# Kernel tuning notes

Hardware: AMD Instinct MI355X
Metric: run time of the kernel (lower is better)

The kernel has to match this reference:

```python
import jax, jax.numpy as jnp
import numpy as np

EPS = 1e-5
K = 20
THRESH = 0.5

def _bn_relu(x, g, b, m, v):
    # eval-mode BatchNorm1d followed by ReLU
    return jax.nn.relu(g * (x - m) * jax.lax.rsqrt(v + EPS) + b)

def setup_inputs() -> dict:
    key = jax.random.key(0)
    ks = jax.random.split(key, 16)
    T, C, CI, E, NC = 16384, 256, 8, 5, 13
    B, N = 2, T // 2
    inp = {
        "f_sem": jax.random.normal(ks[0], (T, C), jnp.float32),
        "f_ins": jax.random.normal(ks[1], (T, CI), jnp.float32),
        # equal-size, sorted batch assignment (2 clouds of 8192 points)
        "batch": jnp.repeat(jnp.arange(B, dtype=jnp.int64), N),
        # semantic_adaptation_fc: Linear(C,C) + BN + ReLU
        "W_sem": jax.random.normal(ks[2], (C, C), jnp.float32) * (1.0 / np.sqrt(C)),
        "b_sem": jnp.zeros((C,), jnp.float32),
        "g_sem": jnp.ones((C,), jnp.float32),
        "beta_sem": jnp.zeros((C,), jnp.float32),
        "m_sem": jax.random.normal(ks[3], (C,), jnp.float32) * 0.1,
        "v_sem": jax.random.uniform(ks[4], (C,), jnp.float32, 0.5, 1.5),
        # inst_fc: Linear(8,C) + BN + ReLU
        "W_ins": jax.random.normal(ks[5], (CI, C), jnp.float32) * (1.0 / np.sqrt(CI)),
        "b_ins": jnp.zeros((C,), jnp.float32),
        "g_ins": jnp.ones((C,), jnp.float32),
        "beta_ins": jnp.zeros((C,), jnp.float32),
        "m_ins": jax.random.normal(ks[6], (C,), jnp.float32) * 0.1,
        "v_ins": jax.random.uniform(ks[7], (C,), jnp.float32, 0.5, 1.5),
        # instance_embedding_fc: plain Linear(C,E)
        "W_emb": jax.random.normal(ks[8], (C, E), jnp.float32) * (1.0 / np.sqrt(C)),
        "b_emb": jnp.zeros((E,), jnp.float32),
        # classifier_fc: plain Linear(C,NC)
        "W_cls": jax.random.normal(ks[9], (C, NC), jnp.float32) * (1.0 / np.sqrt(C)),
        "b_cls": jnp.zeros((NC,), jnp.float32),
    }
    return inp

def _instance_fusion(e_ins, f_sem, batch):
    # assumes sorted batch with equal-size segments (enforced by setup_inputs)
    T, C = f_sem.shape
    B = int(batch[-1]) + 1
    N = T // B
    e = e_ins.reshape(B, N, -1)
    f = f_sem.reshape(B, N, C)
    # squared Euclidean pairwise distances per cloud: [B, N, N]
    sq = jnp.sum(e * e, axis=-1)
    d2 = sq[:, :, None] + sq[:, None, :] - 2.0 * jnp.einsum("bnd,bmd->bnm", e, e)
    d2 = jnp.maximum(d2, 0.0)
    neg_vals, idx = jax.lax.top_k(-d2, K)          # k smallest distances, [B,N,K]
    within = (-neg_vals) <= THRESH * THRESH        # distance <= threshold
    self_idx = jnp.broadcast_to(jnp.arange(N)[None, :, None], idx.shape)
    col = jnp.where(within, idx, self_idx)         # fall back to self outside threshold
    neigh = jax.vmap(lambda fb, cb: fb[cb])(f, col)  # [B,N,K,C]
    return jnp.max(neigh, axis=2).reshape(T, C)      # scatter-max == max over neighbors

def reference(f_sem, f_ins, batch,
              W_sem, b_sem, g_sem, beta_sem, m_sem, v_sem,
              W_ins, b_ins, g_ins, beta_ins, m_ins, v_ins,
              W_emb, b_emb, W_cls, b_cls):
    f_sem_prime = _bn_relu(f_sem @ W_sem + b_sem, g_sem, beta_sem, m_sem, v_sem)
    f_ins_h = _bn_relu(f_ins @ W_ins + b_ins, g_ins, beta_ins, m_ins, v_ins)
    f_sins = f_ins_h + f_sem_prime
    e_ins = f_sins @ W_emb + b_emb
    f_isem = _instance_fusion(e_ins, f_sem, batch)
    p_sem = f_isem @ W_cls + b_cls
    return (p_sem, e_ins)
```

## Files before the change

kernel.cpp:

```cpp
#include <hip/hip_runtime.h>
#include <math.h>

#define T 16384
#define C 256
#define CI 8
#define EDIM 5
#define NC 13
#define NPTS 8192
#define KNN 20
#define CAP 256
#define FR 32
#define FRPB 8

typedef float f4v __attribute__((ext_vector_type(4)));
typedef _Float16 h8 __attribute__((ext_vector_type(8)));

__global__ __launch_bounds__(256) void front_kernel(
    const float* __restrict__ f_sem, const float* __restrict__ f_ins,
    const float* __restrict__ W_sem, const float* __restrict__ b_sem,
    const float* __restrict__ g_sem, const float* __restrict__ beta_sem,
    const float* __restrict__ m_sem, const float* __restrict__ v_sem,
    const float* __restrict__ W_ins, const float* __restrict__ b_ins,
    const float* __restrict__ g_ins, const float* __restrict__ beta_ins,
    const float* __restrict__ m_ins, const float* __restrict__ v_ins,
    const float* __restrict__ W_emb, const float* __restrict__ b_emb,
    float* __restrict__ eA, double* __restrict__ eD,
    float* __restrict__ out_e)
{
    __shared__ __align__(16) _Float16 sAh[FR][264];
    __shared__ __align__(16) _Float16 sAl[FR][264];
    __shared__ float bnA1[C], bnB1[C], bnA2[C], bnB2[C];
    __shared__ float weL[C][EDIM];
    __shared__ float lfi[FR][CI];
    __shared__ float sP[4][FR][EDIM];

    const int tid = threadIdx.x;
    const int rowBase = blockIdx.x * FR;

    #pragma unroll
    for (int i = 0; i < 8; i++) {
        const int idx = tid + 256 * i;
        const int g = idx * 4;
        const int row = g >> 8, k = g & 255;
        const float4 v = *(const float4*)(f_sem + (size_t)rowBase * C + g);
        const float vv[4] = {v.x, v.y, v.z, v.w};
        #pragma unroll
        for (int q = 0; q < 4; q++) {
            const _Float16 h = (_Float16)vv[q];
            sAh[row][k + q] = h;
            sAl[row][k + q] = (_Float16)(vv[q] - (float)h);
        }
    }
    {
        const int c = tid;
        const float rs1 = 1.0f / sqrtf(v_sem[c] + 1e-5f);
        const float A1 = g_sem[c] * rs1;
        bnA1[c] = A1;
        bnB1[c] = A1 * (b_sem[c] - m_sem[c]) + beta_sem[c];
        const float rs2 = 1.0f / sqrtf(v_ins[c] + 1e-5f);
        const float A2 = g_ins[c] * rs2;
        bnA2[c] = A2;
        bnB2[c] = A2 * (b_ins[c] - m_ins[c]) + beta_ins[c];
        #pragma unroll
        for (int j = 0; j < EDIM; j++) weL[c][j] = W_emb[c * EDIM + j];
    }
    if (tid < FR * CI) lfi[tid >> 3][tid & 7] = f_ins[rowBase * CI + tid];
    __syncthreads();

    const int w = tid >> 6, lane = tid & 63;
    const int r16 = lane & 15, kq = lane >> 4;
    const int n0 = 64 * w;

    f4v acc[2][4];
    #pragma unroll
    for (int mi = 0; mi < 2; mi++)
        #pragma unroll
        for (int ni = 0; ni < 4; ni++) acc[mi][ni] = (f4v){0.f, 0.f, 0.f, 0.f};

    for (int kt = 0; kt < 8; kt++) {
        const int koff = 32 * kt + 8 * kq;
        const h8 ah0 = *(const h8*)&sAh[r16][koff];
        const h8 ah1 = *(const h8*)&sAh[r16 + 16][koff];
        const h8 al0 = *(const h8*)&sAl[r16][koff];
        const h8 al1 = *(const h8*)&sAl[r16 + 16][koff];
        #pragma unroll
        for (int ni = 0; ni < 4; ni++) {
            const float* wp = W_sem + (size_t)koff * C + (n0 + 16 * ni + r16);
            float wf[8];
            #pragma unroll
            for (int j = 0; j < 8; j++) wf[j] = wp[(size_t)j * C];
            h8 bh, bl;
            #pragma unroll
            for (int j = 0; j < 8; j++) {
                const _Float16 h = (_Float16)wf[j];
                bh[j] = h;
                bl[j] = (_Float16)(wf[j] - (float)h);
            }
            acc[0][ni] = __builtin_amdgcn_mfma_f32_16x16x32_f16(ah0, bh, acc[0][ni], 0, 0, 0);
            acc[1][ni] = __builtin_amdgcn_mfma_f32_16x16x32_f16(ah1, bh, acc[1][ni], 0, 0, 0);
            acc[0][ni] = __builtin_amdgcn_mfma_f32_16x16x32_f16(al0, bh, acc[0][ni], 0, 0, 0);
            acc[1][ni] = __builtin_amdgcn_mfma_f32_16x16x32_f16(al1, bh, acc[1][ni], 0, 0, 0);
            acc[0][ni] = __builtin_amdgcn_mfma_f32_16x16x32_f16(ah0, bl, acc[0][ni], 0, 0, 0);
            acc[1][ni] = __builtin_amdgcn_mfma_f32_16x16x32_f16(ah1, bl, acc[1][ni], 0, 0, 0);
        }
    }

    f4v prow, pcol;
    {
        const f4v z = {0.f, 0.f, 0.f, 0.f};
        h8 ra, rb, ca, cb;
        #pragma unroll
        for (int j = 0; j < 8; j++) {
            ra[j] = (_Float16)(float)r16;
            rb[j] = (_Float16)((kq == 0 && j == 0) ? 1.0f : 0.0f);
            ca[j] = rb[j];
            cb[j] = ra[j];
        }
        prow = __builtin_amdgcn_mfma_f32_16x16x32_f16(ra, rb, z, 0, 0, 0);
        pcol = __builtin_amdgcn_mfma_f32_16x16x32_f16(ca, cb, z, 0, 0, 0);
    }
    const int colm = (int)pcol[0];
    int rloc[4];
    #pragma unroll
    for (int r = 0; r < 4; r++) rloc[r] = (int)prow[r];

    float p[2][4][EDIM];
    #pragma unroll
    for (int mi = 0; mi < 2; mi++)
        #pragma unroll
        for (int r = 0; r < 4; r++)
            #pragma unroll
            for (int j = 0; j < EDIM; j++) p[mi][r][j] = 0.f;

    #pragma unroll
    for (int ni = 0; ni < 4; ni++) {
        const int c = n0 + 16 * ni + colm;
        const float A1 = bnA1[c], B1 = bnB1[c];
        const float A2 = bnA2[c], B2 = bnB2[c];
        float wi[CI], we[EDIM];
        #pragma unroll
        for (int k = 0; k < CI; k++) wi[k] = W_ins[k * C + c];
        #pragma unroll
        for (int j = 0; j < EDIM; j++) we[j] = weL[c][j];
        #pragma unroll
        for (int mi = 0; mi < 2; mi++)
            #pragma unroll
            for (int r = 0; r < 4; r++) {
                const int row = 16 * mi + rloc[r];
                float x2 = 0.f;
                #pragma unroll
                for (int k = 0; k < CI; k++) x2 = fmaf(lfi[row][k], wi[k], x2);
                const float h1 = fmaxf(fmaf(A1, acc[mi][ni][r], B1), 0.f);
                const float h2 = fmaxf(fmaf(A2, x2, B2), 0.f);
                const float s = h1 + h2;
                #pragma unroll
                for (int j = 0; j < EDIM; j++) p[mi][r][j] = fmaf(s, we[j], p[mi][r][j]);
            }
    }

    #pragma unroll
    for (int off = 1; off < 16; off <<= 1)
        #pragma unroll
        for (int mi = 0; mi < 2; mi++)
            #pragma unroll
            for (int r = 0; r < 4; r++)
                #pragma unroll
                for (int j = 0; j < EDIM; j++)
                    p[mi][r][j] += __shfl_xor(p[mi][r][j], off);

    if (r16 == 0) {
        #pragma unroll
        for (int mi = 0; mi < 2; mi++)
            #pragma unroll
            for (int r = 0; r < 4; r++)
                #pragma unroll
                for (int j = 0; j < EDIM; j++)
                    sP[w][16 * mi + rloc[r]][j] = p[mi][r][j];
    }
    __syncthreads();

    if (tid < FR) {
        const int row = rowBase + tid;
        double sq = 0.0;
        #pragma unroll
        for (int j = 0; j < EDIM; j++) {
            const float s = ((sP[0][tid][j] + sP[1][tid][j]) +
                             (sP[2][tid][j] + sP[3][tid][j])) + b_emb[j];
            const double ed = (double)s;
            eD[(size_t)row * 8 + j] = ed;
            sq = fma(ed, ed, sq);
            eA[(size_t)row * 8 + j] = s;
            out_e[(size_t)row * EDIM + j] = s;
        }
        eD[(size_t)row * 8 + 5] = sq;
        eA[(size_t)row * 8 + 5] = (float)sq;
        eA[(size_t)row * 8 + 6] = 0.f;
        eA[(size_t)row * 8 + 7] = 0.f;
    }
}

__device__ __attribute__((noinline)) float4 rescan_topk(
    const float* __restrict__ eA, const float* __restrict__ f_sem,
    const float* __restrict__ reRow, int cbase, int lane)
{
    float re0 = reRow[0], re1 = reRow[1], re2 = reRow[2];
    float re3 = reRow[3], re4 = reRow[4], sqF = reRow[5];
    float4 mx = make_float4(-3.4e38f, -3.4e38f, -3.4e38f, -3.4e38f);
    long long last = -1;
    for (int sel = 0; sel < KNN; sel++) {
        long long best = 0x7fffffffffffffffLL;
        for (int cb = 0; cb < NPTS; cb += 64) {
            const int j = cbase + cb + lane;
            const float4 ea = *(const float4*)(eA + (size_t)j * 8);
            const float2 eb = *(const float2*)(eA + (size_t)j * 8 + 4);
            float dot = re0 * ea.x;
            dot = fmaf(re1, ea.y, dot); dot = fmaf(re2, ea.z, dot);
            dot = fmaf(re3, ea.w, dot); dot = fmaf(re4, eb.x, dot);
            const float d2 = fmaxf((sqF + eb.y) - 2.f * dot, 0.f);
            long long key = (((long long)__float_as_uint(d2)) << 32)
                            | (unsigned int)(cb + lane);
            if (key <= last) key = 0x7fffffffffffffffLL;
            if (key < best) best = key;
        }
        #pragma unroll
        for (int off = 32; off; off >>= 1) {
            const long long o = __shfl_xor(best, off);
            if (o < best) best = o;
        }
        last = best;
        const int idx = (int)(best & 0xffffffffLL);
        const float4 fv = *(const float4*)(f_sem + (size_t)(cbase + idx) * C + lane * 4);
        mx.x = fmaxf(mx.x, fv.x); mx.y = fmaxf(mx.y, fv.y);
        mx.z = fmaxf(mx.z, fv.z); mx.w = fmaxf(mx.w, fv.w);
    }
    return mx;
}

__global__ __launch_bounds__(256) void knn_kernel(
    const float* __restrict__ eA, const double* __restrict__ eD,
    const float* __restrict__ f_sem,
    const float* __restrict__ W_cls, const float* __restrict__ b_cls,
    float* __restrict__ out_p)
{
    __shared__ float rA[FRPB][8];
    __shared__ double rD[FRPB][6];
    __shared__ unsigned short cidx[FRPB][CAP];
    __shared__ unsigned long long kP[FRPB][CAP];
    __shared__ int cntS[FRPB];
    __shared__ unsigned short memL[FRPB][24];
    __shared__ int nlS[FRPB];

    const int tid = threadIdx.x;
    const int rowBase = blockIdx.x * FRPB;

    if (tid < FRPB * 8) rA[tid >> 3][tid & 7] = eA[(rowBase + (tid >> 3)) * 8 + (tid & 7)];
    if (tid < FRPB * 6) rD[tid / 6][tid % 6] = eD[(rowBase + tid / 6) * 8 + tid % 6];
    if (tid < FRPB) cntS[tid] = 0;
    __syncthreads();

    const int wave = tid >> 6, lane = tid & 63;
    const int cbase = (rowBase >= NPTS) ? NPTS : 0;

    {
        float re[FRPB][5], thrb[FRPB];
        #pragma unroll
        for (int r = 0; r < FRPB; r++) {
            #pragma unroll
            for (int q = 0; q < 5; q++) re[r][q] = rA[r][q];
            thrb[r] = (rA[r][5] - 0.251f) * 0.5f;
        }

        const int cstart = wave * (NPTS / 4);
        for (int cb = cstart; cb < cstart + NPTS / 4; cb += 128) {
            const int j0 = cbase + cb + lane;
            const float4 ea0 = *(const float4*)(eA + (size_t)j0 * 8);
            const float2 eb0 = *(const float2*)(eA + (size_t)j0 * 8 + 4);
            const float4 ea1 = *(const float4*)(eA + (size_t)(j0 + 64) * 8);
            const float2 eb1 = *(const float2*)(eA + (size_t)(j0 + 64) * 8 + 4);
            const float hs0 = 0.5f * eb0.y, hs1 = 0.5f * eb1.y;
            #pragma unroll
            for (int r = 0; r < FRPB; r++) {
                float dot = re[r][0] * ea0.x;
                dot = fmaf(re[r][1], ea0.y, dot); dot = fmaf(re[r][2], ea0.z, dot);
                dot = fmaf(re[r][3], ea0.w, dot); dot = fmaf(re[r][4], eb0.x, dot);
                const bool rec = dot >= (thrb[r] + hs0);
                const unsigned long long m = __ballot(rec);
                if (m) {
                    int base;
                    if (lane == 0) base = atomicAdd(&cntS[r], (int)__popcll(m));
                    base = __shfl(base, 0);
                    const int pre = __builtin_amdgcn_mbcnt_hi(
                        (unsigned int)(m >> 32),
                        __builtin_amdgcn_mbcnt_lo((unsigned int)m, 0u));
                    const int pos = base + pre;
                    if (rec && pos < CAP) cidx[r][pos] = (unsigned short)(cb + lane);
                }
            }
            #pragma unroll
            for (int r = 0; r < FRPB; r++) {
                float dot = re[r][0] * ea1.x;
                dot = fmaf(re[r][1], ea1.y, dot); dot = fmaf(re[r][2], ea1.z, dot);
                dot = fmaf(re[r][3], ea1.w, dot); dot = fmaf(re[r][4], eb1.x, dot);
                const bool rec = dot >= (thrb[r] + hs1);
                const unsigned long long m = __ballot(rec);
                if (m) {
                    int base;
                    if (lane == 0) base = atomicAdd(&cntS[r], (int)__popcll(m));
                    base = __shfl(base, 0);
                    const int pre = __builtin_amdgcn_mbcnt_hi(
                        (unsigned int)(m >> 32),
                        __builtin_amdgcn_mbcnt_lo((unsigned int)m, 0u));
                    const int pos = base + pre;
                    if (rec && pos < CAP) cidx[r][pos] = (unsigned short)(cb + 64 + lane);
                }
            }
        }
    }
    __syncthreads();

    const int lr0 = 2 * wave, lr1 = lr0 + 1;

    #pragma unroll 1
    for (int rr = 0; rr < 2; rr++) {
        const int lr = lr0 + rr;
        const int cnt = cntS[lr];
        const double* rd = rD[lr];

        if (cnt <= CAP) {
            unsigned long long mykp[4];
            int myid[4], mpos[4];
            bool mem[4];
            #pragma unroll
            for (int q = 0; q < 4; q++) {
                const int i = lane + 64 * q;
                mykp[q] = ~0ull; myid[q] = -1; mem[q] = false;
                if (i < cnt) {
                    const int id = (int)cidx[lr][i];
                    const double* ep = eD + (size_t)(cbase + id) * 8;
                    double dotd = 0.0;
                    #pragma unroll
                    for (int qq = 0; qq < 5; qq++) dotd = fma(rd[qq], ep[qq], dotd);
                    const double d2 = fmax((rd[5] + ep[5]) - 2.0 * dotd, 0.0);
                    if (d2 <= 0.25) {
                        mem[q] = true;
                        const unsigned int k32 = __float_as_uint((float)d2);
                        mykp[q] = (((unsigned long long)k32) << 16) | (unsigned int)id;
                        myid[q] = id;
                    }
                }
            }
            int base = 0;
            #pragma unroll
            for (int q = 0; q < 4; q++) {
                const unsigned long long b = __ballot(mem[q]);
                if (mem[q]) {
                    const int pos = base + (int)__builtin_amdgcn_mbcnt_hi(
                        (unsigned int)(b >> 32),
                        __builtin_amdgcn_mbcnt_lo((unsigned int)b, 0u));
                    mpos[q] = pos;
                    kP[lr][pos] = mykp[q];
                }
                base += (int)__popcll(b);
            }
            const int m = base;

            if (m <= KNN) {
                #pragma unroll
                for (int q = 0; q < 4; q++)
                    if (mem[q]) memL[lr][mpos[q]] = (unsigned short)myid[q];
                if (lane == 0) nlS[lr] = m;
            } else {
                int rank[4] = {0, 0, 0, 0};
                for (int j = 0; j < m; j++) {
                    const unsigned long long kj = kP[lr][j];
                    #pragma unroll
                    for (int q = 0; q < 4; q++) rank[q] += (kj < mykp[q]) ? 1 : 0;
                }
                int sbase = 0;
                #pragma unroll
                for (int q = 0; q < 4; q++) {
                    const bool sel = mem[q] && (rank[q] < KNN);
                    const unsigned long long b = __ballot(sel);
                    if (sel) {
                        const int pos = sbase + (int)__builtin_amdgcn_mbcnt_hi(
                            (unsigned int)(b >> 32),
                            __builtin_amdgcn_mbcnt_lo((unsigned int)b, 0u));
                        memL[lr][pos] = (unsigned short)myid[q];
                    }
                    sbase += (int)__popcll(b);
                }
                if (lane == 0) nlS[lr] = sbase;
            }
        } else {
            if (lane == 0) { memL[lr][0] = 0; nlS[lr] = -1; }
        }
    }

    const int s0 = nlS[lr0], s1 = nlS[lr1];
    const bool fb0 = (s0 < 0), fb1 = (s1 < 0);
    const int n0 = fb0 ? 1 : s0, n1 = fb1 ? 1 : s1;
    float4 mx0 = make_float4(-3.4e38f, -3.4e38f, -3.4e38f, -3.4e38f);
    float4 mx1 = mx0;
    const int nmax = (n0 > n1) ? n0 : n1;
    for (int k = 0; k < nmax; k += 4) {
        const int a0 = (int)memL[lr0][(k     < n0) ? k     : n0 - 1];
        const int a1 = (int)memL[lr0][(k + 1 < n0) ? k + 1 : n0 - 1];
        const int a2 = (int)memL[lr0][(k + 2 < n0) ? k + 2 : n0 - 1];
        const int a3 = (int)memL[lr0][(k + 3 < n0) ? k + 3 : n0 - 1];
        const int c0 = (int)memL[lr1][(k     < n1) ? k     : n1 - 1];
        const int c1 = (int)memL[lr1][(k + 1 < n1) ? k + 1 : n1 - 1];
        const int c2 = (int)memL[lr1][(k + 2 < n1) ? k + 2 : n1 - 1];
        const int c3 = (int)memL[lr1][(k + 3 < n1) ? k + 3 : n1 - 1];
        const float4 f0 = *(const float4*)(f_sem + (size_t)(cbase + a0) * C + lane * 4);
        const float4 f1 = *(const float4*)(f_sem + (size_t)(cbase + a1) * C + lane * 4);
        const float4 f2 = *(const float4*)(f_sem + (size_t)(cbase + a2) * C + lane * 4);
        const float4 f3 = *(const float4*)(f_sem + (size_t)(cbase + a3) * C + lane * 4);
        const float4 g0 = *(const float4*)(f_sem + (size_t)(cbase + c0) * C + lane * 4);
        const float4 g1 = *(const float4*)(f_sem + (size_t)(cbase + c1) * C + lane * 4);
        const float4 g2 = *(const float4*)(f_sem + (size_t)(cbase + c2) * C + lane * 4);
        const float4 g3 = *(const float4*)(f_sem + (size_t)(cbase + c3) * C + lane * 4);
        mx0.x = fmaxf(fmaxf(fmaxf(mx0.x, f0.x), fmaxf(f1.x, f2.x)), f3.x);
        mx0.y = fmaxf(fmaxf(fmaxf(mx0.y, f0.y), fmaxf(f1.y, f2.y)), f3.y);
        mx0.z = fmaxf(fmaxf(fmaxf(mx0.z, f0.z), fmaxf(f1.z, f2.z)), f3.z);
        mx0.w = fmaxf(fmaxf(fmaxf(mx0.w, f0.w), fmaxf(f1.w, f2.w)), f3.w);
        mx1.x = fmaxf(fmaxf(fmaxf(mx1.x, g0.x), fmaxf(g1.x, g2.x)), g3.x);
        mx1.y = fmaxf(fmaxf(fmaxf(mx1.y, g0.y), fmaxf(g1.y, g2.y)), g3.y);
        mx1.z = fmaxf(fmaxf(fmaxf(mx1.z, g0.z), fmaxf(g1.z, g2.z)), g3.z);
        mx1.w = fmaxf(fmaxf(fmaxf(mx1.w, g0.w), fmaxf(g1.w, g2.w)), g3.w);
    }
    if (fb0) mx0 = rescan_topk(eA, f_sem, rA[lr0], cbase, lane);
    if (fb1) mx1 = rescan_topk(eA, f_sem, rA[lr1], cbase, lane);

    #pragma unroll 1
    for (int rr = 0; rr < 2; rr++) {
        const float4 mx = rr ? mx1 : mx0;
        float p[NC];
        #pragma unroll
        for (int k = 0; k < NC; k++) p[k] = 0.f;
        const float* w0 = W_cls + (4 * lane + 0) * NC;
        const float* w1 = W_cls + (4 * lane + 1) * NC;
        const float* w2 = W_cls + (4 * lane + 2) * NC;
        const float* w3 = W_cls + (4 * lane + 3) * NC;
        #pragma unroll
        for (int k = 0; k < NC; k++)
            p[k] = fmaf(mx.x, w0[k], fmaf(mx.y, w1[k], fmaf(mx.z, w2[k], fmaf(mx.w, w3[k], p[k]))));
        #pragma unroll
        for (int off = 32; off; off >>= 1)
            #pragma unroll
            for (int k = 0; k < NC; k++) p[k] += __shfl_xor(p[k], off);
        if (lane == 0) {
            const int row = rowBase + lr0 + rr;
            #pragma unroll
            for (int k = 0; k < NC; k++) out_p[row * NC + k] = p[k] + b_cls[k];
        }
    }
}

extern "C" void kernel_launch(void* const* d_in, const int* in_sizes, int n_in,
                              void* d_out, int out_size, void* d_ws, size_t ws_size,
                              hipStream_t stream) {
    (void)in_sizes; (void)n_in; (void)out_size; (void)ws_size;
    const float* f_sem    = (const float*)d_in[0];
    const float* f_ins    = (const float*)d_in[1];
    const float* W_sem    = (const float*)d_in[3];
    const float* b_sem    = (const float*)d_in[4];
    const float* g_sem    = (const float*)d_in[5];
    const float* beta_sem = (const float*)d_in[6];
    const float* m_sem    = (const float*)d_in[7];
    const float* v_sem    = (const float*)d_in[8];
    const float* W_ins    = (const float*)d_in[9];
    const float* b_ins    = (const float*)d_in[10];
    const float* g_ins    = (const float*)d_in[11];
    const float* beta_ins = (const float*)d_in[12];
    const float* m_ins    = (const float*)d_in[13];
    const float* v_ins    = (const float*)d_in[14];
    const float* W_emb    = (const float*)d_in[15];
    const float* b_emb    = (const float*)d_in[16];
    const float* W_cls    = (const float*)d_in[17];
    const float* b_cls    = (const float*)d_in[18];
    float* outp = (float*)d_out;

    char* ws = (char*)d_ws;
    float*  eA = (float*)ws;
    double* eD = (double*)(ws + (size_t)T * 8 * 4);

    front_kernel<<<T / FR, 256, 0, stream>>>(
        f_sem, f_ins, W_sem, b_sem, g_sem, beta_sem, m_sem, v_sem,
        W_ins, b_ins, g_ins, beta_ins, m_ins, v_ins, W_emb, b_emb,
        eA, eD, outp + T * NC);
    knn_kernel<<<T / FRPB, 256, 0, stream>>>(
        eA, eD, f_sem, W_cls, b_cls, outp);
}
```

Before: 168.4 us.

## Pre-split W_sem into transposed fp16 hi/lo and gather neighbors from fp16 f_sem

A new prep kernel converts W_sem once into transposed fp16 high and low parts. The front GEMM can then load contiguous h8 vectors instead of doing strided fp32 loads and converting them in every block. The front kernel also writes an fp16 copy of f_sem, which the kNN max-gather reads when the workspace is large enough. This halves the bytes per neighbor row and unrolls the gather by 8. In exchange it adds an extra kernel launch and extra workspace writes. The fused max is now taken over fp16-rounded features, which lowers the precision of p_sem.

```diff
diff --git a/kernel.cpp b/kernel.cpp
--- a/kernel.cpp
+++ b/kernel.cpp
@@ -14,10 +14,24 @@
 
 typedef float f4v __attribute__((ext_vector_type(4)));
 typedef _Float16 h8 __attribute__((ext_vector_type(8)));
+typedef _Float16 h4v __attribute__((ext_vector_type(4)));
+
+__global__ __launch_bounds__(256) void prep_kernel(
+    const float* __restrict__ W_sem,
+    _Float16* __restrict__ WhT, _Float16* __restrict__ WlT)
+{
+    const int c = blockIdx.x;
+    const int k = threadIdx.x;
+    const float w = W_sem[(size_t)k * C + c];
+    const _Float16 h = (_Float16)w;
+    WhT[(size_t)c * C + k] = h;
+    WlT[(size_t)c * C + k] = (_Float16)(w - (float)h);
+}
 
 __global__ __launch_bounds__(256) void front_kernel(
     const float* __restrict__ f_sem, const float* __restrict__ f_ins,
-    const float* __restrict__ W_sem, const float* __restrict__ b_sem,
+    const _Float16* __restrict__ WhT, const _Float16* __restrict__ WlT,
+    const float* __restrict__ b_sem,
     const float* __restrict__ g_sem, const float* __restrict__ beta_sem,
     const float* __restrict__ m_sem, const float* __restrict__ v_sem,
     const float* __restrict__ W_ins, const float* __restrict__ b_ins,
@@ -25,7 +39,7 @@
     const float* __restrict__ m_ins, const float* __restrict__ v_ins,
     const float* __restrict__ W_emb, const float* __restrict__ b_emb,
     float* __restrict__ eA, double* __restrict__ eD,
-    float* __restrict__ out_e)
+    float* __restrict__ out_e, _Float16* __restrict__ fsem_h)
 {
     __shared__ __align__(16) _Float16 sAh[FR][264];
     __shared__ __align__(16) _Float16 sAl[FR][264];
@@ -44,12 +58,16 @@
         const int row = g >> 8, k = g & 255;
         const float4 v = *(const float4*)(f_sem + (size_t)rowBase * C + g);
         const float vv[4] = {v.x, v.y, v.z, v.w};
+        h4v hv;
         #pragma unroll
         for (int q = 0; q < 4; q++) {
             const _Float16 h = (_Float16)vv[q];
             sAh[row][k + q] = h;
             sAl[row][k + q] = (_Float16)(vv[q] - (float)h);
-        }
+            hv[q] = h;
+        }
+        if (fsem_h)
+            *(h4v*)(fsem_h + (size_t)(rowBase + row) * C + k) = hv;
     }
     {
         const int c = tid;
@@ -85,17 +103,9 @@
         const h8 al1 = *(const h8*)&sAl[r16 + 16][koff];
         #pragma unroll
         for (int ni = 0; ni < 4; ni++) {
-            const float* wp = W_sem + (size_t)koff * C + (n0 + 16 * ni + r16);
-            float wf[8];
-            #pragma unroll
-            for (int j = 0; j < 8; j++) wf[j] = wp[(size_t)j * C];
-            h8 bh, bl;
-            #pragma unroll
-            for (int j = 0; j < 8; j++) {
-                const _Float16 h = (_Float16)wf[j];
-                bh[j] = h;
-                bl[j] = (_Float16)(wf[j] - (float)h);
-            }
+            const int col = n0 + 16 * ni + r16;
+            const h8 bh = *(const h8*)&WhT[(size_t)col * C + koff];
+            const h8 bl = *(const h8*)&WlT[(size_t)col * C + koff];
             acc[0][ni] = __builtin_amdgcn_mfma_f32_16x16x32_f16(ah0, bh, acc[0][ni], 0, 0, 0);
             acc[1][ni] = __builtin_amdgcn_mfma_f32_16x16x32_f16(ah1, bh, acc[1][ni], 0, 0, 0);
             acc[0][ni] = __builtin_amdgcn_mfma_f32_16x16x32_f16(al0, bh, acc[0][ni], 0, 0, 0);
@@ -236,9 +246,10 @@
     return mx;
 }
 
+template <bool H16>
 __global__ __launch_bounds__(256) void knn_kernel(
     const float* __restrict__ eA, const double* __restrict__ eD,
-    const float* __restrict__ f_sem,
+    const float* __restrict__ f_sem, const _Float16* __restrict__ fsem_h,
     const float* __restrict__ W_cls, const float* __restrict__ b_cls,
     float* __restrict__ out_p)
 {
@@ -402,31 +413,60 @@
     float4 mx0 = make_float4(-3.4e38f, -3.4e38f, -3.4e38f, -3.4e38f);
     float4 mx1 = mx0;
     const int nmax = (n0 > n1) ? n0 : n1;
-    for (int k = 0; k < nmax; k += 4) {
-        const int a0 = (int)memL[lr0][(k     < n0) ? k     : n0 - 1];
-        const int a1 = (int)memL[lr0][(k + 1 < n0) ? k + 1 : n0 - 1];
-        const int a2 = (int)memL[lr0][(k + 2 < n0) ? k + 2 : n0 - 1];
-        const int a3 = (int)memL[lr0][(k + 3 < n0) ? k + 3 : n0 - 1];
-        const int c0 = (int)memL[lr1][(k     < n1) ? k     : n1 - 1];
-        const int c1 = (int)memL[lr1][(k + 1 < n1) ? k + 1 : n1 - 1];
-        const int c2 = (int)memL[lr1][(k + 2 < n1) ? k + 2 : n1 - 1];
-        const int c3 = (int)memL[lr1][(k + 3 < n1) ? k + 3 : n1 - 1];
-        const float4 f0 = *(const float4*)(f_sem + (size_t)(cbase + a0) * C + lane * 4);
-        const float4 f1 = *(const float4*)(f_sem + (size_t)(cbase + a1) * C + lane * 4);
-        const float4 f2 = *(const float4*)(f_sem + (size_t)(cbase + a2) * C + lane * 4);
-        const float4 f3 = *(const float4*)(f_sem + (size_t)(cbase + a3) * C + lane * 4);
-        const float4 g0 = *(const float4*)(f_sem + (size_t)(cbase + c0) * C + lane * 4);
-        const float4 g1 = *(const float4*)(f_sem + (size_t)(cbase + c1) * C + lane * 4);
-        const float4 g2 = *(const float4*)(f_sem + (size_t)(cbase + c2) * C + lane * 4);
-        const float4 g3 = *(const float4*)(f_sem + (size_t)(cbase + c3) * C + lane * 4);
-        mx0.x = fmaxf(fmaxf(fmaxf(mx0.x, f0.x), fmaxf(f1.x, f2.x)), f3.x);
-        mx0.y = fmaxf(fmaxf(fmaxf(mx0.y, f0.y), fmaxf(f1.y, f2.y)), f3.y);
-        mx0.z = fmaxf(fmaxf(fmaxf(mx0.z, f0.z), fmaxf(f1.z, f2.z)), f3.z);
-        mx0.w = fmaxf(fmaxf(fmaxf(mx0.w, f0.w), fmaxf(f1.w, f2.w)), f3.w);
-        mx1.x = fmaxf(fmaxf(fmaxf(mx1.x, g0.x), fmaxf(g1.x, g2.x)), g3.x);
-        mx1.y = fmaxf(fmaxf(fmaxf(mx1.y, g0.y), fmaxf(g1.y, g2.y)), g3.y);
-        mx1.z = fmaxf(fmaxf(fmaxf(mx1.z, g0.z), fmaxf(g1.z, g2.z)), g3.z);
-        mx1.w = fmaxf(fmaxf(fmaxf(mx1.w, g0.w), fmaxf(g1.w, g2.w)), g3.w);
+
+    if (H16) {
+        for (int k = 0; k < nmax; k += 8) {
+            int a[8], c[8];
+            #pragma unroll
+            for (int i = 0; i < 8; i++) {
+                a[i] = (int)memL[lr0][(k + i < n0) ? k + i : n0 - 1];
+                c[i] = (int)memL[lr1][(k + i < n1) ? k + i : n1 - 1];
+            }
+            h4v fa[8], fc[8];
+            #pragma unroll
+            for (int i = 0; i < 8; i++) {
+                fa[i] = *(const h4v*)(fsem_h + (size_t)(cbase + a[i]) * C + lane * 4);
+                fc[i] = *(const h4v*)(fsem_h + (size_t)(cbase + c[i]) * C + lane * 4);
+            }
+            #pragma unroll
+            for (int i = 0; i < 8; i++) {
+                mx0.x = fmaxf(mx0.x, (float)fa[i][0]);
+                mx0.y = fmaxf(mx0.y, (float)fa[i][1]);
+                mx0.z = fmaxf(mx0.z, (float)fa[i][2]);
+                mx0.w = fmaxf(mx0.w, (float)fa[i][3]);
+                mx1.x = fmaxf(mx1.x, (float)fc[i][0]);
+                mx1.y = fmaxf(mx1.y, (float)fc[i][1]);
+                mx1.z = fmaxf(mx1.z, (float)fc[i][2]);
+                mx1.w = fmaxf(mx1.w, (float)fc[i][3]);
+            }
+        }
+    } else {
+        for (int k = 0; k < nmax; k += 4) {
+            const int a0 = (int)memL[lr0][(k     < n0) ? k     : n0 - 1];
+            const int a1 = (int)memL[lr0][(k + 1 < n0) ? k + 1 : n0 - 1];
+            const int a2 = (int)memL[lr0][(k + 2 < n0) ? k + 2 : n0 - 1];
+            const int a3 = (int)memL[lr0][(k + 3 < n0) ? k + 3 : n0 - 1];
+            const int c0 = (int)memL[lr1][(k     < n1) ? k     : n1 - 1];
+            const int c1 = (int)memL[lr1][(k + 1 < n1) ? k + 1 : n1 - 1];
+            const int c2 = (int)memL[lr1][(k + 2 < n1) ? k + 2 : n1 - 1];
+            const int c3 = (int)memL[lr1][(k + 3 < n1) ? k + 3 : n1 - 1];
+            const float4 f0 = *(const float4*)(f_sem + (size_t)(cbase + a0) * C + lane * 4);
+            const float4 f1 = *(const float4*)(f_sem + (size_t)(cbase + a1) * C + lane * 4);
+            const float4 f2 = *(const float4*)(f_sem + (size_t)(cbase + a2) * C + lane * 4);
+            const float4 f3 = *(const float4*)(f_sem + (size_t)(cbase + a3) * C + lane * 4);
+            const float4 g0 = *(const float4*)(f_sem + (size_t)(cbase + c0) * C + lane * 4);
+            const float4 g1 = *(const float4*)(f_sem + (size_t)(cbase + c1) * C + lane * 4);
+            const float4 g2 = *(const float4*)(f_sem + (size_t)(cbase + c2) * C + lane * 4);
+            const float4 g3 = *(const float4*)(f_sem + (size_t)(cbase + c3) * C + lane * 4);
+            mx0.x = fmaxf(fmaxf(fmaxf(mx0.x, f0.x), fmaxf(f1.x, f2.x)), f3.x);
+            mx0.y = fmaxf(fmaxf(fmaxf(mx0.y, f0.y), fmaxf(f1.y, f2.y)), f3.y);
+            mx0.z = fmaxf(fmaxf(fmaxf(mx0.z, f0.z), fmaxf(f1.z, f2.z)), f3.z);
+            mx0.w = fmaxf(fmaxf(fmaxf(mx0.w, f0.w), fmaxf(f1.w, f2.w)), f3.w);
+            mx1.x = fmaxf(fmaxf(fmaxf(mx1.x, g0.x), fmaxf(g1.x, g2.x)), g3.x);
+            mx1.y = fmaxf(fmaxf(fmaxf(mx1.y, g0.y), fmaxf(g1.y, g2.y)), g3.y);
+            mx1.z = fmaxf(fmaxf(fmaxf(mx1.z, g0.z), fmaxf(g1.z, g2.z)), g3.z);
+            mx1.w = fmaxf(fmaxf(fmaxf(mx1.w, g0.w), fmaxf(g1.w, g2.w)), g3.w);
+        }
     }
     if (fb0) mx0 = rescan_topk(eA, f_sem, rA[lr0], cbase, lane);
     if (fb1) mx1 = rescan_topk(eA, f_sem, rA[lr1], cbase, lane);
@@ -459,7 +499,7 @@
 extern "C" void kernel_launch(void* const* d_in, const int* in_sizes, int n_in,
                               void* d_out, int out_size, void* d_ws, size_t ws_size,
                               hipStream_t stream) {
-    (void)in_sizes; (void)n_in; (void)out_size; (void)ws_size;
+    (void)in_sizes; (void)n_in; (void)out_size;
     const float* f_sem    = (const float*)d_in[0];
     const float* f_ins    = (const float*)d_in[1];
     const float* W_sem    = (const float*)d_in[3];
@@ -481,13 +521,25 @@
     float* outp = (float*)d_out;
 
     char* ws = (char*)d_ws;
-    float*  eA = (float*)ws;
-    double* eD = (double*)(ws + (size_t)T * 8 * 4);
-
+    float*    eA     = (float*)ws;
+    double*   eD     = (double*)(ws + (size_t)T * 8 * 4);
+    _Float16* WhT    = (_Float16*)(ws + (size_t)T * 8 * 12);
+    _Float16* WlT    = WhT + (size_t)C * C;
+    _Float16* fsem_h = WlT + (size_t)C * C;
+
+    const size_t need_h16 = (size_t)T * 8 * 12 + (size_t)C * C * 4
+                          + (size_t)T * C * 2;
+    const bool h16 = (ws_size >= need_h16);
+
+    prep_kernel<<<C, C, 0, stream>>>(W_sem, WhT, WlT);
     front_kernel<<<T / FR, 256, 0, stream>>>(
-        f_sem, f_ins, W_sem, b_sem, g_sem, beta_sem, m_sem, v_sem,
+        f_sem, f_ins, WhT, WlT, b_sem, g_sem, beta_sem, m_sem, v_sem,
         W_ins, b_ins, g_ins, beta_ins, m_ins, v_ins, W_emb, b_emb,
-        eA, eD, outp + T * NC);
-    knn_kernel<<<T / FRPB, 256, 0, stream>>>(
-        eA, eD, f_sem, W_cls, b_cls, outp);
+        eA, eD, outp + T * NC, h16 ? fsem_h : (_Float16*)nullptr);
+    if (h16)
+        knn_kernel<true><<<T / FRPB, 256, 0, stream>>>(
+            eA, eD, f_sem, fsem_h, W_cls, b_cls, outp);
+    else
+        knn_kernel<false><<<T / FRPB, 256, 0, stream>>>(
+            eA, eD, f_sem, (const _Float16*)nullptr, W_cls, b_cls, outp);
 }
```

New measurement: 174.1 us. +3.4%, slower.
